# Kernel optimization log

Hardware: AMD Instinct MI355X
Metric: run time of the kernel (lower is better)

## Reference

```python
import jax, jax.numpy as jnp
import numpy as np

TEMPERATURE = 0.2
NUM_CLASSES = 80  # background label == NUM_CLASSES
M, K, B = 8192, 128, 60


def setup_inputs() -> dict:
    key = jax.random.key(0)
    k1, k2, k3 = jax.random.split(key, 3)
    feats = jax.random.normal(k1, (M, K), dtype=jnp.float32)
    feats = feats / jnp.linalg.norm(feats, axis=-1, keepdims=True)
    protos = jax.random.normal(k2, (B, K), dtype=jnp.float32)
    protos = protos / jnp.linalg.norm(protos, axis=-1, keepdims=True)
    labels = jax.random.randint(k3, (M,), 0, NUM_CLASSES + 1)  # NUM_CLASSES == bg
    proto_labels = jnp.arange(B, dtype=jnp.int64 if jax.config.read('jax_enable_x64') else jnp.int32)
    return {"features": feats, "labels": labels, "protos": protos, "proto_labels": proto_labels}


def reference(features, labels, protos, proto_labels):
    # masked (fixed-shape) formulation of the original boolean-gather code
    fg = labels != NUM_CLASSES                                   # [M]
    is_base = fg & jnp.any(labels[None, :] == proto_labels[:, None], axis=0)
    is_novel = fg & ~is_base
    nf = is_novel.astype(features.dtype)                         # [M] novel mask
    bf = is_base.astype(features.dtype)                          # [M] base mask
    numel = jnp.sum(fg).astype(features.dtype)

    sim = jnp.matmul(features, features.T) / TEMPERATURE          # [M,M]
    pk = jnp.matmul(features, protos.T) / TEMPERATURE             # [M,B]
    exp_sim = jnp.exp(sim)                                        # [M,M]
    eye = jnp.eye(features.shape[0], dtype=features.dtype)
    offdiag = (1.0 - eye)

    # ---- novel branch: rows i with is_novel[i] ----
    # denom: sum over novel j != i of exp(sim) + sum over protos of RAW pk (faithful to source)
    exp_nn_sum = jnp.sum(exp_sim * nf[None, :] * offdiag, axis=1)  # [M]
    denom_n = exp_nn_sum + jnp.sum(pk, axis=1)                     # [M]
    log_prob = sim - jnp.log(denom_n)[:, None]
    # novel_label_mask in source is elementwise labels==labels -> all True
    n_novel = jnp.sum(nf)
    cnt = jnp.maximum(n_novel - 1.0, 1.0)                          # per-row positive count
    per_row_novel = -jnp.sum(log_prob * nf[None, :] * offdiag, axis=1) / cnt
    loss_novel = jnp.sum(per_row_novel * nf)
    loss_novel = jnp.where(n_novel > 1.0, loss_novel, 0.0)

    # ---- base branch: rows i with is_base[i] ----
    safe_lab = jnp.clip(labels, 0, protos.shape[0] - 1)
    pi = jnp.einsum('nc,nc->n', features, protos[safe_lab]) / TEMPERATURE  # [M]
    denom_b = jnp.sum(exp_sim * nf[None, :], axis=1) + jnp.sum(jnp.exp(pk), axis=1)
    loss_base = jnp.sum(bf * -(pi - jnp.log(denom_b)))
    loss_base = jnp.where(jnp.any(is_base), loss_base, 0.0)

    return (loss_novel + loss_base) / numel
```

## Files before the change

kernel.cpp:

```cpp
#include <hip/hip_runtime.h>
#include <math.h>

#define NCLS 80
#define KDIM 128
#define INV_T 5.0f

typedef __attribute__((ext_vector_type(4))) float  floatx4;
typedef __attribute__((ext_vector_type(8))) short  short8;

__device__ inline unsigned short f2bf(float x) {
    unsigned int u = __float_as_uint(x);
    u += 0x7fffu + ((u >> 16) & 1u);
    return (unsigned short)(u >> 16);
}
__device__ inline short8 pack8(float4 a, float4 b) {
    short8 o;
    o[0] = (short)f2bf(a.x); o[1] = (short)f2bf(a.y);
    o[2] = (short)f2bf(a.z); o[3] = (short)f2bf(a.w);
    o[4] = (short)f2bf(b.x); o[5] = (short)f2bf(b.y);
    o[6] = (short)f2bf(b.z); o[7] = (short)f2bf(b.w);
    return o;
}
__device__ inline void g2lds16(const void* g, void* l) {
    __builtin_amdgcn_global_load_lds(
        (const __attribute__((address_space(1))) void*)g,
        (__attribute__((address_space(3))) void*)l, 16, 0, 0);
}

__global__ __launch_bounds__(256) void setup_kernel(
    const float* __restrict__ feats, const int* __restrict__ labels,
    const float* __restrict__ protos, int M, int B,
    int* __restrict__ novel_idx, int* __restrict__ counters,
    float* __restrict__ accz,
    float* __restrict__ out,
    unsigned short* __restrict__ Fb, unsigned short* __restrict__ Pb)
{
    const int i = blockIdx.x * 256 + threadIdx.x;
    const int T = gridDim.x * 256;
    if (i == 0) out[0] = 0.f;
    if (i < M) {
        int lab = labels[i];
        bool fg  = (lab != NCLS);
        bool isb = fg && (lab >= 0) && (lab < B);
        bool isn = fg && !isb;
        if (isn) { int p = atomicAdd(&counters[0], 1); novel_idx[p] = i; }
        if (fg)  atomicAdd(&counters[1], 1);
        if (isb) atomicAdd(&counters[2], 1);
    }
    if (i < M) *((float4*)accz + i) = make_float4(0.f, 0.f, 0.f, 0.f);

    const int nch = (M + 1) * (KDIM / 8);
    for (int ch = i; ch < nch; ch += T) {
        short8 o = (short8)0;
        if (ch < M * (KDIM / 8)) {
            const float4* f4 = (const float4*)feats + (size_t)ch * 2;
            o = pack8(f4[0], f4[1]);
        }
        *(short8*)&Fb[(size_t)ch * 8] = o;
    }
    if (i < 128 * (KDIM / 8)) {
        int r = i >> 4;
        short8 o = (short8)0;
        if (r < B) {
            const float4* p4 = (const float4*)protos + (size_t)i * 2;
            o = pack8(p4[0], p4[1]);
        }
        *(short8*)&Pb[(size_t)i * 8] = o;
    }
}

__device__ inline void flush_run(float se16[4][4], float sr16[4][4],
                                 float* dE, float* dR, int row0,
                                 int wrow, int quad, int lr, int M)
{
    #pragma unroll
    for (int r = 0; r < 4; ++r) {
        #pragma unroll
        for (int reg = 0; reg < 4; ++reg) {
            float ve = se16[r][reg], vr = sr16[r][reg];
            #pragma unroll
            for (int off = 1; off < 16; off <<= 1) {
                ve += __shfl_xor(ve, off);
                vr += __shfl_xor(vr, off);
            }
            if (lr == 0) {
                int irow = row0 + wrow + r * 16 + quad * 4 + reg;
                if (irow < M) { atomicAdd(&dE[irow], ve); atomicAdd(&dR[irow], vr); }
            }
        }
    }
}

__global__ __launch_bounds__(256, 2) void gemm_kernel(
    const unsigned short* __restrict__ Fb, const unsigned short* __restrict__ Pb,
    const int* __restrict__ novel_idx, const int* __restrict__ counters,
    int M, int B,
    float* __restrict__ S1, float* __restrict__ T1,
    float* __restrict__ PKr, float* __restrict__ EK)
{
    __shared__ unsigned short As[128 * 128];
    __shared__ unsigned short Bs[128 * 128];
    __shared__ int nidx[128];

    const int Nn = counters[0];
    const int ntiles = (Nn + 127) >> 7;
    const int width = ntiles + 1;
    const int rtc = (M + 127) >> 7;
    const long total = (long)rtc * width;
    const int G = gridDim.x, b = blockIdx.x;
    const int t0 = (int)(total * b / G);
    const int t1 = (int)(total * (b + 1) / G);
    if (t0 >= t1) return;

    const int tid = threadIdx.x;
    const int wbase = tid & ~63;
    const int wave = tid >> 6, lane = tid & 63;
    const int lr = lane & 15, quad = lane >> 4;
    const int wrow = (wave >> 1) * 64, wcol = (wave & 1) * 64;

    float se16[4][4], sr16[4][4];
    int pend_row0 = -1;
    bool pend_isp = false;
    int cur_rt = -1;
    bool first = true;

    for (int t = t0; t < t1; ++t) {
        const int rt = t / width, ct = t - rt * width;
        const bool isp = (ct == ntiles);
        const int row0 = rt * 128;

        if (isp != pend_isp || row0 != pend_row0) {
            if (pend_row0 >= 0)
                flush_run(se16, sr16, pend_isp ? EK : S1, pend_isp ? PKr : T1,
                          pend_row0, wrow, quad, lr, M);
            #pragma unroll
            for (int r = 0; r < 4; ++r)
                #pragma unroll
                for (int g = 0; g < 4; ++g) { se16[r][g] = 0.f; sr16[r][g] = 0.f; }
            pend_isp = isp; pend_row0 = row0;
        }

        if (!first) __syncthreads();
        first = false;

        if (rt != cur_rt) {
            cur_rt = rt;
            const unsigned short* a0 = Fb + (size_t)row0 * KDIM;
            #pragma unroll
            for (int p = 0; p < 8; ++p) {
                int Lc = p * 256 + tid;
                int r = Lc >> 4, c = Lc & 15;
                int cs = c ^ (r & 15);
                g2lds16(a0 + (size_t)r * KDIM + cs * 8,
                        As + (size_t)(p * 256 + wbase) * 8);
            }
        }
        #pragma unroll
        for (int p = 0; p < 8; ++p) {
            int Lc = p * 256 + tid;
            int r = Lc >> 4, c = Lc & 15;
            int cs = c ^ (r & 15);
            const unsigned short* base; int nid;
            if (isp) { base = Pb; nid = r; }
            else {
                base = Fb;
                int jg = ct * 128 + r;
                nid = (jg < Nn) ? novel_idx[jg] : M;
            }
            g2lds16(base + (size_t)nid * KDIM + cs * 8,
                    Bs + (size_t)(p * 256 + wbase) * 8);
        }
        if (tid < 128) {
            int nid = -1;
            if (isp) { if (tid < B) nid = tid; }
            else { int jg = ct * 128 + tid; if (jg < Nn) nid = novel_idx[jg]; }
            nidx[tid] = nid;
        }
        __syncthreads();

        floatx4 acc[4][4];
        #pragma unroll
        for (int r = 0; r < 4; ++r)
            #pragma unroll
            for (int c = 0; c < 4; ++c)
                acc[r][c] = (floatx4){0.f, 0.f, 0.f, 0.f};

        #pragma unroll
        for (int ks = 0; ks < 4; ++ks) {
            short8 a[4], bfr[4];
            #pragma unroll
            for (int r = 0; r < 4; ++r) {
                int row = wrow + r * 16 + lr;
                int phys = (ks * 4 + quad) ^ lr;
                a[r] = *(const short8*)&As[row * KDIM + phys * 8];
            }
            #pragma unroll
            for (int c = 0; c < 4; ++c) {
                int row = wcol + c * 16 + lr;
                int phys = (ks * 4 + quad) ^ lr;
                bfr[c] = *(const short8*)&Bs[row * KDIM + phys * 8];
            }
            #pragma unroll
            for (int r = 0; r < 4; ++r)
                #pragma unroll
                for (int c = 0; c < 4; ++c)
                    acc[r][c] = __builtin_amdgcn_mfma_f32_16x16x32_bf16(
                        a[r], bfr[c], acc[r][c], 0, 0, 0);
        }

        int ncol[4];
        #pragma unroll
        for (int c = 0; c < 4; ++c) ncol[c] = nidx[wcol + c * 16 + lr];
        #pragma unroll
        for (int r = 0; r < 4; ++r) {
            int ibase = row0 + wrow + r * 16 + quad * 4;
            #pragma unroll
            for (int reg = 0; reg < 4; ++reg) {
                int irow = ibase + reg;
                float se = 0.f, sr = 0.f;
                #pragma unroll
                for (int c = 0; c < 4; ++c) {
                    float sim = acc[r][c][reg] * INV_T;
                    bool valid = (ncol[c] >= 0) && (isp || ncol[c] != irow);
                    if (valid) { se += __expf(sim); sr += sim; }
                }
                se16[r][reg] += se;
                sr16[r][reg] += sr;
            }
        }
    }
    if (pend_row0 >= 0)
        flush_run(se16, sr16, pend_isp ? EK : S1, pend_isp ? PKr : T1,
                  pend_row0, wrow, quad, lr, M);
}

__global__ __launch_bounds__(256) void finalize_kernel(
    const float* __restrict__ feats, const float* __restrict__ protos,
    const int* __restrict__ labels,
    const float* __restrict__ S1, const float* __restrict__ T1,
    const float* __restrict__ PKr, const float* __restrict__ EK,
    const int* __restrict__ counters, int M, int B, float* __restrict__ out)
{
    __shared__ float part[16];
    const int tid  = threadIdx.x;
    const int rloc = tid >> 4;
    const int q    = tid & 15;
    const int row  = blockIdx.x * 16 + rloc;
    const int rs   = min(row, M - 1);

    const int Nn = counters[0], numel = counters[1], nbase = counters[2];

    int lab = labels[rs];
    bool fg  = (lab != NCLS);
    bool isb = fg && (lab >= 0) && (lab < B);
    bool isn = fg && !isb;
    int  sl  = min(max(lab, 0), B - 1);

    const float4* f4 = (const float4*)(feats  + (size_t)rs * KDIM) + q * 2;
    const float4* p4 = (const float4*)(protos + (size_t)sl * KDIM) + q * 2;
    float4 a0 = f4[0], a1 = f4[1];
    float4 b0 = p4[0], b1 = p4[1];
    float d = a0.x * b0.x + a0.y * b0.y + a0.z * b0.z + a0.w * b0.w
            + a1.x * b1.x + a1.y * b1.y + a1.z * b1.z + a1.w * b1.w;
    #pragma unroll
    for (int off = 1; off < 16; off <<= 1) d += __shfl_xor(d, off);

    if (q == 0) {
        float loss = 0.f;
        if (row < M) {
            if (isn && Nn > 1) {
                float cnt = (float)(Nn - 1);
                float dn  = S1[rs] + PKr[rs];
                loss = -(T1[rs] - cnt * logf(dn)) / cnt;
            } else if (isb && nbase > 0) {
                float pi = d * INV_T;
                float db = S1[rs] + EK[rs];
                loss = -(pi - logf(db));
            }
        }
        part[rloc] = loss;
    }
    __syncthreads();
    if (tid == 0) {
        float s = 0.f;
        #pragma unroll
        for (int r = 0; r < 16; ++r) s += part[r];
        atomicAdd(out, s / (float)numel);
    }
}

extern "C" void kernel_launch(void* const* d_in, const int* in_sizes, int n_in,
                              void* d_out, int out_size, void* d_ws, size_t ws_size,
                              hipStream_t stream)
{
    const float* feats  = (const float*)d_in[0];
    const int*   labels = (const int*)d_in[1];
    const float* protos = (const float*)d_in[2];

    const int M = in_sizes[1];
    const int B = in_sizes[3];

    char* ws = (char*)d_ws;
    int*   counters = (int*)ws;
    float* S1  = (float*)(ws + 64);
    float* T1  = S1 + M;
    float* PKr = T1 + M;
    float* EK  = PKr + M;
    int*   novel_idx = (int*)(EK + M);
    unsigned short* Fb = (unsigned short*)(novel_idx + M);
    unsigned short* Pb = Fb + (size_t)(M + 1) * KDIM;

    hipMemsetAsync(counters, 0, 64, stream);

    setup_kernel<<<512, 256, 0, stream>>>(
        feats, labels, protos, M, B, novel_idx, counters,
        S1, (float*)d_out, Fb, Pb);

    gemm_kernel<<<512, 256, 0, stream>>>(
        Fb, Pb, novel_idx, counters, M, B, S1, T1, PKr, EK);

    finalize_kernel<<<(M + 15) / 16, 256, 0, stream>>>(
        feats, protos, labels, S1, T1, PKr, EK, counters, M, B, (float*)d_out);
}
```

Measured before the change: 99.31 us.

## Fuse setup, GEMM and finalize into one cooperative kernel with grid syncs

```diff
diff --git a/kernel.cpp b/kernel.cpp
--- a/kernel.cpp
+++ b/kernel.cpp
@@ -1,5 +1,8 @@
 #include <hip/hip_runtime.h>
+#include <hip/hip_cooperative_groups.h>
 #include <math.h>
+
+namespace cg = cooperative_groups;
 
 #define NCLS 80
 #define KDIM 128
@@ -27,7 +30,9 @@
         (__attribute__((address_space(3))) void*)l, 16, 0, 0);
 }
 
-__global__ __launch_bounds__(256) void setup_kernel(
+
+__device__ inline void dev_setup(
+    int gi, int T,
     const float* __restrict__ feats, const int* __restrict__ labels,
     const float* __restrict__ protos, int M, int B,
     int* __restrict__ novel_idx, int* __restrict__ counters,
@@ -35,22 +40,19 @@
     float* __restrict__ out,
     unsigned short* __restrict__ Fb, unsigned short* __restrict__ Pb)
 {
-    const int i = blockIdx.x * 256 + threadIdx.x;
-    const int T = gridDim.x * 256;
-    if (i == 0) out[0] = 0.f;
-    if (i < M) {
-        int lab = labels[i];
+    if (gi == 0) out[0] = 0.f;
+    if (gi < M) {
+        int lab = labels[gi];
         bool fg  = (lab != NCLS);
         bool isb = fg && (lab >= 0) && (lab < B);
         bool isn = fg && !isb;
-        if (isn) { int p = atomicAdd(&counters[0], 1); novel_idx[p] = i; }
+        if (isn) { int p = atomicAdd(&counters[0], 1); novel_idx[p] = gi; }
         if (fg)  atomicAdd(&counters[1], 1);
         if (isb) atomicAdd(&counters[2], 1);
-    }
-    if (i < M) *((float4*)accz + i) = make_float4(0.f, 0.f, 0.f, 0.f);
-
+        *((float4*)accz + gi) = make_float4(0.f, 0.f, 0.f, 0.f);
+    }
     const int nch = (M + 1) * (KDIM / 8);
-    for (int ch = i; ch < nch; ch += T) {
+    for (int ch = gi; ch < nch; ch += T) {
         short8 o = (short8)0;
         if (ch < M * (KDIM / 8)) {
             const float4* f4 = (const float4*)feats + (size_t)ch * 2;
@@ -58,14 +60,14 @@
         }
         *(short8*)&Fb[(size_t)ch * 8] = o;
     }
-    if (i < 128 * (KDIM / 8)) {
-        int r = i >> 4;
+    if (gi < 128 * (KDIM / 8)) {
+        int r = gi >> 4;
         short8 o = (short8)0;
         if (r < B) {
-            const float4* p4 = (const float4*)protos + (size_t)i * 2;
+            const float4* p4 = (const float4*)protos + (size_t)gi * 2;
             o = pack8(p4[0], p4[1]);
         }
-        *(short8*)&Pb[(size_t)i * 8] = o;
+        *(short8*)&Pb[(size_t)gi * 8] = o;
     }
 }
 
@@ -91,28 +93,24 @@
     }
 }
 
-__global__ __launch_bounds__(256, 2) void gemm_kernel(
+__device__ inline void dev_gemm(
+    unsigned short* As, unsigned short* Bs, int* nidx,
+    int G, int b, int tid,
     const unsigned short* __restrict__ Fb, const unsigned short* __restrict__ Pb,
     const int* __restrict__ novel_idx, const int* __restrict__ counters,
     int M, int B,
     float* __restrict__ S1, float* __restrict__ T1,
     float* __restrict__ PKr, float* __restrict__ EK)
 {
-    __shared__ unsigned short As[128 * 128];
-    __shared__ unsigned short Bs[128 * 128];
-    __shared__ int nidx[128];
-
     const int Nn = counters[0];
     const int ntiles = (Nn + 127) >> 7;
     const int width = ntiles + 1;
     const int rtc = (M + 127) >> 7;
     const long total = (long)rtc * width;
-    const int G = gridDim.x, b = blockIdx.x;
     const int t0 = (int)(total * b / G);
     const int t1 = (int)(total * (b + 1) / G);
     if (t0 >= t1) return;
 
-    const int tid = threadIdx.x;
     const int wbase = tid & ~63;
     const int wave = tid >> 6, lane = tid & 63;
     const int lr = lane & 15, quad = lane >> 4;
@@ -234,18 +232,17 @@
                   pend_row0, wrow, quad, lr, M);
 }
 
-__global__ __launch_bounds__(256) void finalize_kernel(
+__device__ inline void dev_finalize(
+    float* part, int blk, int tid,
     const float* __restrict__ feats, const float* __restrict__ protos,
     const int* __restrict__ labels,
     const float* __restrict__ S1, const float* __restrict__ T1,
     const float* __restrict__ PKr, const float* __restrict__ EK,
     const int* __restrict__ counters, int M, int B, float* __restrict__ out)
 {
-    __shared__ float part[16];
-    const int tid  = threadIdx.x;
     const int rloc = tid >> 4;
     const int q    = tid & 15;
-    const int row  = blockIdx.x * 16 + rloc;
+    const int row  = blk * 16 + rloc;
     const int rs   = min(row, M - 1);
 
     const int Nn = counters[0], numel = counters[1], nbase = counters[2];
@@ -289,6 +286,73 @@
     }
 }
 
+__global__ __launch_bounds__(256, 2) void fused_kernel(
+    const float* __restrict__ feats, const int* __restrict__ labels,
+    const float* __restrict__ protos, int M, int B,
+    int* __restrict__ novel_idx, int* __restrict__ counters,
+    float* __restrict__ S1, float* __restrict__ T1,
+    float* __restrict__ PKr, float* __restrict__ EK,
+    unsigned short* __restrict__ Fb, unsigned short* __restrict__ Pb,
+    float* __restrict__ out)
+{
+    __shared__ unsigned short As[128 * 128];
+    __shared__ unsigned short Bs[128 * 128];
+    __shared__ int nidx[128];
+    __shared__ float part[16];
+
+    cg::grid_group grid = cg::this_grid();
+    const int tid = threadIdx.x;
+    const int gi  = blockIdx.x * 256 + tid;
+    const int T   = gridDim.x * 256;
+
+    dev_setup(gi, T, feats, labels, protos, M, B, novel_idx, counters,
+              S1, out, Fb, Pb);
+    grid.sync();
+    dev_gemm(As, Bs, nidx, gridDim.x, blockIdx.x, tid,
+             Fb, Pb, novel_idx, counters, M, B, S1, T1, PKr, EK);
+    grid.sync();
+    dev_finalize(part, blockIdx.x, tid, feats, protos, labels,
+                 S1, T1, PKr, EK, counters, M, B, out);
+}
+
+__global__ __launch_bounds__(256) void setup_kernel(
+    const float* __restrict__ feats, const int* __restrict__ labels,
+    const float* __restrict__ protos, int M, int B,
+    int* __restrict__ novel_idx, int* __restrict__ counters,
+    float* __restrict__ accz, float* __restrict__ out,
+    unsigned short* __restrict__ Fb, unsigned short* __restrict__ Pb)
+{
+    dev_setup(blockIdx.x * 256 + threadIdx.x, gridDim.x * 256,
+              feats, labels, protos, M, B, novel_idx, counters,
+              accz, out, Fb, Pb);
+}
+
+__global__ __launch_bounds__(256, 2) void gemm_kernel(
+    const unsigned short* __restrict__ Fb, const unsigned short* __restrict__ Pb,
+    const int* __restrict__ novel_idx, const int* __restrict__ counters,
+    int M, int B,
+    float* __restrict__ S1, float* __restrict__ T1,
+    float* __restrict__ PKr, float* __restrict__ EK)
+{
+    __shared__ unsigned short As[128 * 128];
+    __shared__ unsigned short Bs[128 * 128];
+    __shared__ int nidx[128];
+    dev_gemm(As, Bs, nidx, gridDim.x, blockIdx.x, threadIdx.x,
+             Fb, Pb, novel_idx, counters, M, B, S1, T1, PKr, EK);
+}
+
+__global__ __launch_bounds__(256) void finalize_kernel(
+    const float* __restrict__ feats, const float* __restrict__ protos,
+    const int* __restrict__ labels,
+    const float* __restrict__ S1, const float* __restrict__ T1,
+    const float* __restrict__ PKr, const float* __restrict__ EK,
+    const int* __restrict__ counters, int M, int B, float* __restrict__ out)
+{
+    __shared__ float part[16];
+    dev_finalize(part, blockIdx.x, threadIdx.x, feats, protos, labels,
+                 S1, T1, PKr, EK, counters, M, B, out);
+}
+
 extern "C" void kernel_launch(void* const* d_in, const int* in_sizes, int n_in,
                               void* d_out, int out_size, void* d_ws, size_t ws_size,
                               hipStream_t stream)
@@ -297,8 +361,8 @@
     const int*   labels = (const int*)d_in[1];
     const float* protos = (const float*)d_in[2];
 
-    const int M = in_sizes[1];
-    const int B = in_sizes[3];
+    int M = in_sizes[1];
+    int B = in_sizes[3];
 
     char* ws = (char*)d_ws;
     int*   counters = (int*)ws;
@@ -312,13 +376,23 @@
 
     hipMemsetAsync(counters, 0, 64, stream);
 
-    setup_kernel<<<512, 256, 0, stream>>>(
-        feats, labels, protos, M, B, novel_idx, counters,
-        S1, (float*)d_out, Fb, Pb);
-
-    gemm_kernel<<<512, 256, 0, stream>>>(
-        Fb, Pb, novel_idx, counters, M, B, S1, T1, PKr, EK);
-
-    finalize_kernel<<<(M + 15) / 16, 256, 0, stream>>>(
-        feats, protos, labels, S1, T1, PKr, EK, counters, M, B, (float*)d_out);
-}
+    float* outp = (float*)d_out;
+    void* kargs[] = {
+        (void*)&feats, (void*)&labels, (void*)&protos,
+        (void*)&M, (void*)&B,
+        (void*)&novel_idx, (void*)&counters,
+        (void*)&S1, (void*)&T1, (void*)&PKr, (void*)&EK,
+        (void*)&Fb, (void*)&Pb, (void*)&outp
+    };
+    hipError_t e = hipLaunchCooperativeKernel(
+        (const void*)fused_kernel, dim3(512), dim3(256), kargs, 0, stream);
+    if (e != hipSuccess) {
+        setup_kernel<<<512, 256, 0, stream>>>(
+            feats, labels, protos, M, B, novel_idx, counters,
+            S1, outp, Fb, Pb);
+        gemm_kernel<<<512, 256, 0, stream>>>(
+            Fb, Pb, novel_idx, counters, M, B, S1, T1, PKr, EK);
+        finalize_kernel<<<(M + 15) / 16, 256, 0, stream>>>(
+            feats, protos, labels, S1, T1, PKr, EK, counters, M, B, outp);
+    }
+}
```

Result: slower. 222.9 us (+124.5%).
